# Optimization experiments

Measured on AMD Instinct MI355X. Metric: run time of the kernel, lower is better.

## Reference

```python
import jax, jax.numpy as jnp
import numpy as np

B, S, D, H = 2, 2048, 1024, 16
DK = D // H

def setup_inputs() -> dict:
    key = jax.random.key(0)
    ks = jax.random.split(key, 9)
    scale = 1.0 / np.sqrt(D)
    return {
        "x": jax.random.normal(ks[0], (B, S, D), dtype=jnp.float32),
        "Wq": jax.random.uniform(ks[1], (D, D), jnp.float32, -scale, scale),
        "bq": jax.random.uniform(ks[2], (D,), jnp.float32, -scale, scale),
        "Wk": jax.random.uniform(ks[3], (D, D), jnp.float32, -scale, scale),
        "bk": jax.random.uniform(ks[4], (D,), jnp.float32, -scale, scale),
        "Wv": jax.random.uniform(ks[5], (D, D), jnp.float32, -scale, scale),
        "bv": jax.random.uniform(ks[6], (D,), jnp.float32, -scale, scale),
        "Wo": jax.random.uniform(ks[7], (D, D), jnp.float32, -scale, scale),
        "bo": jax.random.uniform(ks[8], (D,), jnp.float32, -scale, scale),
    }

def reference(x, Wq, bq, Wk, bk, Wv, bv, Wo, bo):
    # QKV projections (torch Linear: x @ W.T + b)
    q = x @ Wq.T + bq
    k = x @ Wk.T + bk
    v = x @ Wv.T + bv
    # [B, H, S, DK]
    q = q.reshape(B, S, H, DK).transpose(0, 2, 1, 3)
    k = k.reshape(B, S, H, DK).transpose(0, 2, 1, 3)
    v = v.reshape(B, S, H, DK).transpose(0, 2, 1, 3)
    scores = jnp.einsum('bhqd,bhkd->bhqk', q, k) / jnp.sqrt(jnp.float32(DK))
    p = jax.nn.softmax(scores, axis=-1)  # dropout is identity in eval mode
    o = jnp.einsum('bhqk,bhkd->bhqd', p, v)
    o = o.transpose(0, 2, 1, 3).reshape(B, S, D)
    return o @ Wo.T + bo
```

## Files before the change

### kernel.cpp

```cpp
#include <hip/hip_runtime.h>
#include <hip/hip_bf16.h>


typedef __attribute__((ext_vector_type(8))) short short8;
typedef __attribute__((ext_vector_type(4))) float f32x4;
typedef __attribute__((ext_vector_type(4))) unsigned int u32x4;
typedef __attribute__((ext_vector_type(8))) unsigned short u16x8;

__device__ __forceinline__ unsigned short f2bf(float f) {
    unsigned int u = __builtin_bit_cast(unsigned int, f);
    u += 0x7FFFu + ((u >> 16) & 1u);
    return (unsigned short)(u >> 16);
}

__device__ __forceinline__ unsigned short bfc(float f) {
    return __builtin_bit_cast(unsigned short, __float2bfloat16(f));
}

__device__ __forceinline__ float exp2_fast(float x) {
    return __builtin_amdgcn_exp2f(x);
}

__device__ __forceinline__ void gload16(const void* gsrc, void* ldst) {
    __builtin_amdgcn_global_load_lds(
        (const __attribute__((address_space(1))) unsigned int*)gsrc,
        (__attribute__((address_space(3))) unsigned int*)ldst, 16, 0, 0);
}

__global__ void cast_all(const float* __restrict__ x,
                         const float* __restrict__ wq, const float* __restrict__ wk,
                         const float* __restrict__ wv, const float* __restrict__ wo,
                         unsigned short* __restrict__ xb,
                         unsigned short* __restrict__ wqb, unsigned short* __restrict__ wkb,
                         unsigned short* __restrict__ wvb, unsigned short* __restrict__ wob)
{
    const int bid = blockIdx.x;
    const float* src; unsigned short* dst; int i;
    if (bid < 4096) {
        src = x; dst = xb; i = bid * 256 + threadIdx.x;
    } else {
        int t = (bid - 4096) >> 10;
        int lb = (bid - 4096) & 1023;
        src = (t == 0) ? wq : (t == 1) ? wk : (t == 2) ? wv : wo;
        dst = (t == 0) ? wqb : (t == 1) ? wkb : (t == 2) ? wvb : wob;
        i = lb * 256 + threadIdx.x;
    }
    float4 v = reinterpret_cast<const float4*>(src)[i];
    ushort4 o;
    o.x = f2bf(v.x); o.y = f2bf(v.y); o.z = f2bf(v.z); o.w = f2bf(v.w);
    reinterpret_cast<ushort4*>(dst)[i] = o;
}

__global__ __launch_bounds__(256, 2)
void qkv_gemm(const unsigned short* __restrict__ A,
              const unsigned short* __restrict__ Wq_,
              const unsigned short* __restrict__ Wk_,
              const unsigned short* __restrict__ Wv_,
              const float* __restrict__ bq_,
              const float* __restrict__ bk_,
              const float* __restrict__ bv_,
              unsigned short* __restrict__ Qb,
              unsigned short* __restrict__ Kb,
              unsigned short* __restrict__ Vtb)
{
    const int K = 1024;
    __shared__ __align__(16) unsigned short As[128][64];
    __shared__ __align__(16) unsigned short Bs[128][64];

    const int lid = blockIdx.x + 8 * blockIdx.y + 256 * blockIdx.z;
    const int xcd = lid & 7;
    const int j   = lid >> 3;
    const int z   = j >> 5;
    const int rr  = j & 31;
    const int by  = xcd * 4 + (rr >> 3);
    const int bx  = rr & 7;

    const unsigned short* Bw = (z == 0) ? Wq_ : (z == 1) ? Wk_ : Wv_;
    const float* bias = (z == 0) ? bq_ : (z == 1) ? bk_ : bv_;
    unsigned short* dst = (z == 0) ? Qb : (z == 1) ? Kb : Vtb;
    const float alpha = (z == 0) ? 0.125f * 1.44269504088896340736f : 1.0f;

    const int tid  = threadIdx.x;
    const int lane = tid & 63;
    const int wave = tid >> 6;
    const int wm = (wave >> 1) * 64;
    const int wn = (wave & 1) * 64;
    const int rowBase = by * 128;
    const int colBase = bx * 128;
    const int l15 = lane & 15;
    const int lg  = lane >> 4;

    const int srow   = lane >> 3;
    const int schunk = lane & 7;
    const int gchunk = schunk ^ srow;

    f32x4 acc[4][4] = {};

    for (int kt = 0; kt < K; kt += 64) {
        __syncthreads();
#pragma unroll
        for (int it = 0; it < 4; ++it) {
            int r = wave * 8 + it * 32 + srow;
            gload16(A  + (size_t)(rowBase + r) * K + kt + gchunk * 8, &As[wave * 8 + it * 32][0]);
            gload16(Bw + (size_t)(colBase + r) * K + kt + gchunk * 8, &Bs[wave * 8 + it * 32][0]);
        }
        __syncthreads();
#pragma unroll
        for (int kk = 0; kk < 2; ++kk) {
            short8 af[4], bf[4];
#pragma unroll
            for (int fm = 0; fm < 4; ++fm) {
                int r  = wm + fm * 16 + l15;
                int kb = (kk * 4 + lg) ^ (r & 7);
                af[fm] = *reinterpret_cast<const short8*>(&As[r][kb * 8]);
            }
#pragma unroll
            for (int fn = 0; fn < 4; ++fn) {
                int r  = wn + fn * 16 + l15;
                int kb = (kk * 4 + lg) ^ (r & 7);
                bf[fn] = *reinterpret_cast<const short8*>(&Bs[r][kb * 8]);
            }
#pragma unroll
            for (int fm = 0; fm < 4; ++fm)
#pragma unroll
                for (int fn = 0; fn < 4; ++fn)
                    acc[fm][fn] = __builtin_amdgcn_mfma_f32_16x16x32_bf16(
                        af[fm], bf[fn], acc[fm][fn], 0, 0, 0);
        }
    }

#pragma unroll
    for (int fm = 0; fm < 4; ++fm)
#pragma unroll
        for (int fn = 0; fn < 4; ++fn)
#pragma unroll
            for (int r = 0; r < 4; ++r) {
                int grow = rowBase + wm + fm * 16 + lg * 4 + r;
                int gcol = colBase + wn + fn * 16 + l15;
                float v = (acc[fm][fn][r] + bias[gcol]) * alpha;
                int b = grow >> 11, s = grow & 2047;
                int h = gcol >> 6,  dk = gcol & 63;
                if (z < 2)
                    dst[(((size_t)b * 16 + h) * 2048 + s) * 64 + dk] = f2bf(v);
                else
                    dst[(((size_t)b * 16 + h) * 64 + dk) * 2048 + s] = f2bf(v);
            }
}

__global__ __launch_bounds__(256, 2)
void gemm_out(const unsigned short* __restrict__ A,
              const unsigned short* __restrict__ Bw,
              const float* __restrict__ bias,
              float* __restrict__ Cout, int M, int N, int K)
{
    __shared__ __align__(16) unsigned short As[128][64];
    __shared__ __align__(16) unsigned short Bs[64][64];

    const int lid = blockIdx.x + 16 * blockIdx.y;
    const int xcd = lid & 7;
    const int j   = lid >> 3;
    const int by  = xcd * 4 + (j >> 4);
    const int bx  = j & 15;

    const int tid  = threadIdx.x;
    const int lane = tid & 63;
    const int wave = tid >> 6;
    const int wm = (wave >> 1) * 64;
    const int wn = (wave & 1) * 32;
    const int rowBase = by * 128;
    const int colBase = bx * 64;
    const int l15 = lane & 15;
    const int lg  = lane >> 4;

    const int srow   = lane >> 3;
    const int schunk = lane & 7;
    const int gchunk = schunk ^ srow;

    f32x4 acc[4][2] = {};

    for (int kt = 0; kt < K; kt += 64) {
        __syncthreads();
#pragma unroll
        for (int it = 0; it < 4; ++it) {
            int r = wave * 8 + it * 32 + srow;
            gload16(A + (size_t)(rowBase + r) * K + kt + gchunk * 8, &As[wave * 8 + it * 32][0]);
        }
#pragma unroll
        for (int it = 0; it < 2; ++it) {
            int rb = wave * 16 + it * 8;
            int r  = rb + srow;
            gload16(Bw + (size_t)(colBase + r) * K + kt + gchunk * 8, &Bs[rb][0]);
        }
        __syncthreads();
#pragma unroll
        for (int kk = 0; kk < 2; ++kk) {
            short8 af[4], bf[2];
#pragma unroll
            for (int fm = 0; fm < 4; ++fm) {
                int r  = wm + fm * 16 + l15;
                int kb = (kk * 4 + lg) ^ (r & 7);
                af[fm] = *reinterpret_cast<const short8*>(&As[r][kb * 8]);
            }
#pragma unroll
            for (int fn = 0; fn < 2; ++fn) {
                int r  = wn + fn * 16 + l15;
                int kb = (kk * 4 + lg) ^ (r & 7);
                bf[fn] = *reinterpret_cast<const short8*>(&Bs[r][kb * 8]);
            }
#pragma unroll
            for (int fm = 0; fm < 4; ++fm)
#pragma unroll
                for (int fn = 0; fn < 2; ++fn)
                    acc[fm][fn] = __builtin_amdgcn_mfma_f32_16x16x32_bf16(
                        af[fm], bf[fn], acc[fm][fn], 0, 0, 0);
        }
    }

#pragma unroll
    for (int fm = 0; fm < 4; ++fm)
#pragma unroll
        for (int fn = 0; fn < 2; ++fn)
#pragma unroll
            for (int r = 0; r < 4; ++r) {
                int grow = rowBase + wm + fm * 16 + lg * 4 + r;
                int gcol = colBase + wn + fn * 16 + l15;
                Cout[(size_t)grow * N + gcol] = acc[fm][fn][r] + bias[gcol];
            }
}

__global__ __launch_bounds__(256, 2)
void attn_kernel(const unsigned short* __restrict__ Q,
                 const unsigned short* __restrict__ Kt,
                 const unsigned short* __restrict__ Vt,
                 unsigned short* __restrict__ O)
{
    __shared__ __align__(16) unsigned short Ks[2][128][64];
    __shared__ __align__(16) unsigned short Vs[2][64][128];

    const int lid = blockIdx.x + 16 * blockIdx.y;
    const int bh  = 4 * (lid & 7) + ((lid >> 3) & 3);
    const int qt  = lid >> 5;
    const int tid  = threadIdx.x;
    const int lane = tid & 63;
    const int w    = tid >> 6;
    const int l15 = lane & 15;
    const int lg  = lane >> 4;

    const unsigned short* Qbh = Q  + (size_t)bh * 2048 * 64;
    const unsigned short* Kbh = Kt + (size_t)bh * 2048 * 64;
    const unsigned short* Vbh = Vt + (size_t)bh * 64 * 2048;

    short8 qf[2][2];
#pragma unroll
    for (int fq = 0; fq < 2; ++fq)
#pragma unroll
        for (int kk = 0; kk < 2; ++kk) {
            int row = qt * 128 + w * 32 + fq * 16 + l15;
            qf[fq][kk] = *reinterpret_cast<const short8*>(
                Qbh + (size_t)row * 64 + kk * 32 + lg * 8);
        }

    short8 ones;
#pragma unroll
    for (int j = 0; j < 8; ++j) ones[j] = (short)0x3F80;

    f32x4 accO[2][4] = {};
    f32x4 accSum[2] = {};

    const int sr  = tid >> 3, skb = tid & 7;
    const int vr  = tid >> 4, vkb = tid & 15;

    u16x8 kst[4], vst[4];
#pragma unroll
    for (int it = 0; it < 4; ++it)
        kst[it] = *reinterpret_cast<const u16x8*>(Kbh + (size_t)(sr + it * 32) * 64 + skb * 8);
#pragma unroll
    for (int it = 0; it < 4; ++it)
        vst[it] = *reinterpret_cast<const u16x8*>(Vbh + (size_t)(vr + it * 16) * 2048 + vkb * 8);

    int cur = 0;
    for (int t = 0; t < 16; ++t) {
#pragma unroll
        for (int it = 0; it < 4; ++it) {
            int r = sr + it * 32;
            *reinterpret_cast<u16x8*>(&Ks[cur][r][(skb ^ (r & 7)) * 8]) = kst[it];
        }
#pragma unroll
        for (int it = 0; it < 4; ++it) {
            int r = vr + it * 16;
            *reinterpret_cast<u16x8*>(&Vs[cur][r][(vkb ^ (r & 15)) * 8]) = vst[it];
        }
        __syncthreads();

        if (t < 15) {
#pragma unroll
            for (int it = 0; it < 4; ++it)
                kst[it] = *reinterpret_cast<const u16x8*>(
                    Kbh + (size_t)((t + 1) * 128 + sr + it * 32) * 64 + skb * 8);
#pragma unroll
            for (int it = 0; it < 4; ++it)
                vst[it] = *reinterpret_cast<const u16x8*>(
                    Vbh + (size_t)(vr + it * 16) * 2048 + (t + 1) * 128 + vkb * 8);
        }

        f32x4 accS[8][2] = {};
#pragma unroll
        for (int kk = 0; kk < 2; ++kk) {
            short8 kf[8];
#pragma unroll
            for (int fk = 0; fk < 8; ++fk) {
                int r  = fk * 16 + l15;
                int kb = (kk * 4 + lg) ^ (r & 7);
                kf[fk] = *reinterpret_cast<const short8*>(&Ks[cur][r][kb * 8]);
            }
#pragma unroll
            for (int fk = 0; fk < 8; ++fk)
#pragma unroll
                for (int fq = 0; fq < 2; ++fq)
                    accS[fk][fq] = __builtin_amdgcn_mfma_f32_16x16x32_bf16(
                        kf[fk], qf[fq][kk], accS[fk][fq], 0, 0, 0);
        }

#pragma unroll
        for (int hh = 0; hh < 2; ++hh) {
            unsigned int plo[2][4], phi[2][4];
#pragma unroll
            for (int fq = 0; fq < 2; ++fq)
#pragma unroll
                for (int f2 = 0; f2 < 4; ++f2) {
                    int fk = hh * 4 + f2;
                    float p0 = exp2_fast(accS[fk][fq][0]);
                    float p1 = exp2_fast(accS[fk][fq][1]);
                    float p2 = exp2_fast(accS[fk][fq][2]);
                    float p3 = exp2_fast(accS[fk][fq][3]);
                    plo[fq][f2] = (unsigned int)bfc(p0) | ((unsigned int)bfc(p1) << 16);
                    phi[fq][f2] = (unsigned int)bfc(p2) | ((unsigned int)bfc(p3) << 16);
                }

#pragma unroll
            for (int k2 = 0; k2 < 2; ++k2) {
                short8 vf[4];
#pragma unroll
                for (int fd = 0; fd < 4; ++fd) {
                    int row = fd * 16 + l15;
                    int kb  = ((hh * 2 + k2) * 4 + lg) ^ (row & 15);
                    vf[fd] = *reinterpret_cast<const short8*>(&Vs[cur][row][kb * 8]);
                }
#pragma unroll
                for (int fq = 0; fq < 2; ++fq) {
                    unsigned int Alo = plo[fq][2 * k2], Blo = plo[fq][2 * k2 + 1];
                    auto r1 = __builtin_amdgcn_permlane32_swap(Alo, Blo, false, false);
                    auto r2 = __builtin_amdgcn_permlane16_swap(r1[0], r1[1], false, false);
                    unsigned int Ahi = phi[fq][2 * k2], Bhi = phi[fq][2 * k2 + 1];
                    auto r3 = __builtin_amdgcn_permlane32_swap(Ahi, Bhi, false, false);
                    auto r4 = __builtin_amdgcn_permlane16_swap(r3[0], r3[1], false, false);
                    u32x4 fw;
                    fw[0] = r2[0];
                    fw[1] = r4[0];
                    fw[2] = r2[1];
                    fw[3] = r4[1];
                    short8 pf = __builtin_bit_cast(short8, fw);
#pragma unroll
                    for (int fd = 0; fd < 4; ++fd)
                        accO[fq][fd] = __builtin_amdgcn_mfma_f32_16x16x32_bf16(
                            pf, vf[fd], accO[fq][fd], 0, 0, 0);
                    accSum[fq] = __builtin_amdgcn_mfma_f32_16x16x32_bf16(
                        pf, ones, accSum[fq], 0, 0, 0);
                }
            }
        }

        cur ^= 1;
    }

    const int b = bh >> 4, h = bh & 15;
#pragma unroll
    for (int fq = 0; fq < 2; ++fq)
#pragma unroll
        for (int r = 0; r < 4; ++r) {
            float linv = 1.0f / accSum[fq][r];
            int s = qt * 128 + w * 32 + fq * 16 + lg * 4 + r;
#pragma unroll
            for (int fd = 0; fd < 4; ++fd) {
                int dk = fd * 16 + l15;
                O[((size_t)b * 2048 + s) * 1024 + h * 64 + dk] = f2bf(accO[fq][fd][r] * linv);
            }
        }
}

extern "C" void kernel_launch(void* const* d_in, const int* in_sizes, int n_in,
                              void* d_out, int out_size, void* d_ws, size_t ws_size,
                              hipStream_t stream)
{
    const float* x  = (const float*)d_in[0];
    const float* Wq = (const float*)d_in[1];
    const float* bq = (const float*)d_in[2];
    const float* Wk = (const float*)d_in[3];
    const float* bk = (const float*)d_in[4];
    const float* Wv = (const float*)d_in[5];
    const float* bv = (const float*)d_in[6];
    const float* Wo = (const float*)d_in[7];
    const float* bo = (const float*)d_in[8];
    float* out = (float*)d_out;

    char* ws = (char*)d_ws;
    unsigned short* xb  = (unsigned short*)(ws);
    unsigned short* wqb = (unsigned short*)(ws + ((size_t)8  << 20));
    unsigned short* wkb = (unsigned short*)(ws + ((size_t)10 << 20));
    unsigned short* wvb = (unsigned short*)(ws + ((size_t)12 << 20));
    unsigned short* wob = (unsigned short*)(ws + ((size_t)14 << 20));
    unsigned short* Qb  = (unsigned short*)(ws + ((size_t)16 << 20));
    unsigned short* Kb  = (unsigned short*)(ws + ((size_t)24 << 20));
    unsigned short* Vtb = (unsigned short*)(ws + ((size_t)32 << 20));
    unsigned short* Ob  = (unsigned short*)(ws + ((size_t)40 << 20));

    cast_all<<<8192, 256, 0, stream>>>(x, Wq, Wk, Wv, Wo,
                                       xb, wqb, wkb, wvb, wob);

    qkv_gemm<<<dim3(8, 32, 3), 256, 0, stream>>>(xb, wqb, wkb, wvb, bq, bk, bv,
                                                 Qb, Kb, Vtb);

    attn_kernel<<<dim3(16, 32), 256, 0, stream>>>(Qb, Kb, Vtb, Ob);

    gemm_out<<<dim3(16, 32), 256, 0, stream>>>(Ob, wob, bo, out, 4096, 1024, 1024);
}
```

Baseline: 109.0 us.

## Software-pipeline attention loop so PV of previous tile overlaps QK^T of current

The attention main loop is restructured so each step computes QK^T and the exp/pack for key tile t while running the P·V MFMAs for tile t-1, using ping-pong register buffers for the packed probabilities. The goal is to interleave the exp (transcendental) work with independent MFMA work so the matrix units stay busy instead of waiting on the softmax. The cost is doubled P register storage, which adds register pressure and may lower occupancy, plus an extra barrier per step to protect the double-buffered LDS.

```diff
diff --git a/kernel.cpp b/kernel.cpp
--- a/kernel.cpp
+++ b/kernel.cpp
@@ -266,112 +266,149 @@
 
     f32x4 accO[2][4] = {};
     f32x4 accSum[2] = {};
+    f32x4 accS[8][2];
 
     const int sr  = tid >> 3, skb = tid & 7;
     const int vr  = tid >> 4, vkb = tid & 15;
 
     u16x8 kst[4], vst[4];
-#pragma unroll
-    for (int it = 0; it < 4; ++it)
-        kst[it] = *reinterpret_cast<const u16x8*>(Kbh + (size_t)(sr + it * 32) * 64 + skb * 8);
-#pragma unroll
-    for (int it = 0; it < 4; ++it)
-        vst[it] = *reinterpret_cast<const u16x8*>(Vbh + (size_t)(vr + it * 16) * 2048 + vkb * 8);
-
-    int cur = 0;
-    for (int t = 0; t < 16; ++t) {
-#pragma unroll
-        for (int it = 0; it < 4; ++it) {
-            int r = sr + it * 32;
-            *reinterpret_cast<u16x8*>(&Ks[cur][r][(skb ^ (r & 7)) * 8]) = kst[it];
-        }
-#pragma unroll
-        for (int it = 0; it < 4; ++it) {
-            int r = vr + it * 16;
-            *reinterpret_cast<u16x8*>(&Vs[cur][r][(vkb ^ (r & 15)) * 8]) = vst[it];
-        }
-        __syncthreads();
-
-        if (t < 15) {
-#pragma unroll
-            for (int it = 0; it < 4; ++it)
-                kst[it] = *reinterpret_cast<const u16x8*>(
-                    Kbh + (size_t)((t + 1) * 128 + sr + it * 32) * 64 + skb * 8);
-#pragma unroll
-            for (int it = 0; it < 4; ++it)
-                vst[it] = *reinterpret_cast<const u16x8*>(
-                    Vbh + (size_t)(vr + it * 16) * 2048 + (t + 1) * 128 + vkb * 8);
-        }
-
-        f32x4 accS[8][2] = {};
-#pragma unroll
-        for (int kk = 0; kk < 2; ++kk) {
-            short8 kf[8];
-#pragma unroll
-            for (int fk = 0; fk < 8; ++fk) {
-                int r  = fk * 16 + l15;
-                int kb = (kk * 4 + lg) ^ (r & 7);
-                kf[fk] = *reinterpret_cast<const short8*>(&Ks[cur][r][kb * 8]);
-            }
-#pragma unroll
-            for (int fk = 0; fk < 8; ++fk)
-#pragma unroll
-                for (int fq = 0; fq < 2; ++fq)
-                    accS[fk][fq] = __builtin_amdgcn_mfma_f32_16x16x32_bf16(
-                        kf[fk], qf[fq][kk], accS[fk][fq], 0, 0, 0);
-        }
-
-#pragma unroll
-        for (int hh = 0; hh < 2; ++hh) {
-            unsigned int plo[2][4], phi[2][4];
-#pragma unroll
-            for (int fq = 0; fq < 2; ++fq)
-#pragma unroll
-                for (int f2 = 0; f2 < 4; ++f2) {
-                    int fk = hh * 4 + f2;
-                    float p0 = exp2_fast(accS[fk][fq][0]);
-                    float p1 = exp2_fast(accS[fk][fq][1]);
-                    float p2 = exp2_fast(accS[fk][fq][2]);
-                    float p3 = exp2_fast(accS[fk][fq][3]);
-                    plo[fq][f2] = (unsigned int)bfc(p0) | ((unsigned int)bfc(p1) << 16);
-                    phi[fq][f2] = (unsigned int)bfc(p2) | ((unsigned int)bfc(p3) << 16);
-                }
-
-#pragma unroll
-            for (int k2 = 0; k2 < 2; ++k2) {
-                short8 vf[4];
-#pragma unroll
-                for (int fd = 0; fd < 4; ++fd) {
-                    int row = fd * 16 + l15;
-                    int kb  = ((hh * 2 + k2) * 4 + lg) ^ (row & 15);
-                    vf[fd] = *reinterpret_cast<const short8*>(&Vs[cur][row][kb * 8]);
-                }
-#pragma unroll
-                for (int fq = 0; fq < 2; ++fq) {
-                    unsigned int Alo = plo[fq][2 * k2], Blo = plo[fq][2 * k2 + 1];
-                    auto r1 = __builtin_amdgcn_permlane32_swap(Alo, Blo, false, false);
-                    auto r2 = __builtin_amdgcn_permlane16_swap(r1[0], r1[1], false, false);
-                    unsigned int Ahi = phi[fq][2 * k2], Bhi = phi[fq][2 * k2 + 1];
-                    auto r3 = __builtin_amdgcn_permlane32_swap(Ahi, Bhi, false, false);
-                    auto r4 = __builtin_amdgcn_permlane16_swap(r3[0], r3[1], false, false);
-                    u32x4 fw;
-                    fw[0] = r2[0];
-                    fw[1] = r4[0];
-                    fw[2] = r2[1];
-                    fw[3] = r4[1];
-                    short8 pf = __builtin_bit_cast(short8, fw);
-#pragma unroll
-                    for (int fd = 0; fd < 4; ++fd)
-                        accO[fq][fd] = __builtin_amdgcn_mfma_f32_16x16x32_bf16(
-                            pf, vf[fd], accO[fq][fd], 0, 0, 0);
-                    accSum[fq] = __builtin_amdgcn_mfma_f32_16x16x32_bf16(
-                        pf, ones, accSum[fq], 0, 0, 0);
-                }
-            }
-        }
-
-        cur ^= 1;
-    }
+    unsigned int PAlo[2][2][4], PAhi[2][2][4];
+    unsigned int PBlo[2][2][4], PBhi[2][2][4];
+
+#define GLOAD(T)                                                              \
+    {                                                                         \
+        _Pragma("unroll")                                                     \
+        for (int it = 0; it < 4; ++it)                                        \
+            kst[it] = *reinterpret_cast<const u16x8*>(                        \
+                Kbh + (size_t)((T) * 128 + sr + it * 32) * 64 + skb * 8);     \
+        _Pragma("unroll")                                                     \
+        for (int it = 0; it < 4; ++it)                                        \
+            vst[it] = *reinterpret_cast<const u16x8*>(                        \
+                Vbh + (size_t)(vr + it * 16) * 2048 + (T) * 128 + vkb * 8);   \
+    }
+
+#define WRITE_T(BT)                                                           \
+    {                                                                         \
+        _Pragma("unroll")                                                     \
+        for (int it = 0; it < 4; ++it) {                                      \
+            int r = sr + it * 32;                                             \
+            *reinterpret_cast<u16x8*>(&Ks[BT][r][(skb ^ (r & 7)) * 8]) = kst[it]; \
+        }                                                                     \
+        _Pragma("unroll")                                                     \
+        for (int it = 0; it < 4; ++it) {                                      \
+            int r = vr + it * 16;                                             \
+            *reinterpret_cast<u16x8*>(&Vs[BT][r][(vkb ^ (r & 15)) * 8]) = vst[it]; \
+        }                                                                     \
+    }
+
+#define QKT_T(BT)                                                             \
+    {                                                                         \
+        _Pragma("unroll")                                                     \
+        for (int fk = 0; fk < 8; ++fk)                                        \
+            _Pragma("unroll")                                                 \
+            for (int fq = 0; fq < 2; ++fq) accS[fk][fq] = f32x4{};            \
+        _Pragma("unroll")                                                     \
+        for (int kk = 0; kk < 2; ++kk) {                                      \
+            short8 kf[8];                                                     \
+            _Pragma("unroll")                                                 \
+            for (int fk = 0; fk < 8; ++fk) {                                  \
+                int r  = fk * 16 + l15;                                       \
+                int kb = (kk * 4 + lg) ^ (r & 7);                             \
+                kf[fk] = *reinterpret_cast<const short8*>(&Ks[BT][r][kb * 8]);\
+            }                                                                 \
+            _Pragma("unroll")                                                 \
+            for (int fk = 0; fk < 8; ++fk)                                    \
+                _Pragma("unroll")                                             \
+                for (int fq = 0; fq < 2; ++fq)                                \
+                    accS[fk][fq] = __builtin_amdgcn_mfma_f32_16x16x32_bf16(   \
+                        kf[fk], qf[fq][kk], accS[fk][fq], 0, 0, 0);           \
+        }                                                                     \
+    }
+
+#define PACK_T(PClo, PChi)                                                    \
+    {                                                                         \
+        _Pragma("unroll")                                                     \
+        for (int hh = 0; hh < 2; ++hh)                                        \
+            _Pragma("unroll")                                                 \
+            for (int fq = 0; fq < 2; ++fq)                                    \
+                _Pragma("unroll")                                             \
+                for (int f2 = 0; f2 < 4; ++f2) {                              \
+                    int fk = hh * 4 + f2;                                     \
+                    float p0 = exp2_fast(accS[fk][fq][0]);                    \
+                    float p1 = exp2_fast(accS[fk][fq][1]);                    \
+                    float p2 = exp2_fast(accS[fk][fq][2]);                    \
+                    float p3 = exp2_fast(accS[fk][fq][3]);                    \
+                    PClo[hh][fq][f2] = (unsigned int)bfc(p0) | ((unsigned int)bfc(p1) << 16); \
+                    PChi[hh][fq][f2] = (unsigned int)bfc(p2) | ((unsigned int)bfc(p3) << 16); \
+                }                                                             \
+    }
+
+#define PV_PREV(BV, PPlo, PPhi)                                               \
+    {                                                                         \
+        _Pragma("unroll")                                                     \
+        for (int hh = 0; hh < 2; ++hh)                                        \
+            _Pragma("unroll")                                                 \
+            for (int k2 = 0; k2 < 2; ++k2) {                                  \
+                short8 vf[4];                                                 \
+                _Pragma("unroll")                                             \
+                for (int fd = 0; fd < 4; ++fd) {                              \
+                    int row = fd * 16 + l15;                                  \
+                    int kb  = ((hh * 2 + k2) * 4 + lg) ^ (row & 15);          \
+                    vf[fd] = *reinterpret_cast<const short8*>(&Vs[BV][row][kb * 8]); \
+                }                                                             \
+                _Pragma("unroll")                                             \
+                for (int fq = 0; fq < 2; ++fq) {                              \
+                    unsigned int Alo = PPlo[hh][fq][2 * k2], Blo = PPlo[hh][fq][2 * k2 + 1]; \
+                    auto r1 = __builtin_amdgcn_permlane32_swap(Alo, Blo, false, false); \
+                    auto r2 = __builtin_amdgcn_permlane16_swap(r1[0], r1[1], false, false); \
+                    unsigned int Ahi = PPhi[hh][fq][2 * k2], Bhi = PPhi[hh][fq][2 * k2 + 1]; \
+                    auto r3 = __builtin_amdgcn_permlane32_swap(Ahi, Bhi, false, false); \
+                    auto r4 = __builtin_amdgcn_permlane16_swap(r3[0], r3[1], false, false); \
+                    u32x4 fw;                                                 \
+                    fw[0] = r2[0]; fw[1] = r4[0]; fw[2] = r2[1]; fw[3] = r4[1]; \
+                    short8 pf = __builtin_bit_cast(short8, fw);               \
+                    _Pragma("unroll")                                         \
+                    for (int fd = 0; fd < 4; ++fd)                            \
+                        accO[fq][fd] = __builtin_amdgcn_mfma_f32_16x16x32_bf16( \
+                            pf, vf[fd], accO[fq][fd], 0, 0, 0);               \
+                    accSum[fq] = __builtin_amdgcn_mfma_f32_16x16x32_bf16(     \
+                        pf, ones, accSum[fq], 0, 0, 0);                       \
+                }                                                             \
+            }                                                                 \
+    }
+
+#define STEP(T, BT, PPlo, PPhi, PClo, PChi)                                   \
+    {                                                                         \
+        WRITE_T(BT);                                                          \
+        __syncthreads();                                                      \
+        if ((T) < 15) { GLOAD((T) + 1); }                                     \
+        QKT_T(BT);                                                            \
+        PV_PREV(BT ^ 1, PPlo, PPhi);                                          \
+        PACK_T(PClo, PChi);                                                   \
+        __syncthreads();                                                      \
+    }
+
+    GLOAD(0);
+    WRITE_T(0);
+    __syncthreads();
+    GLOAD(1);
+    QKT_T(0);
+    PACK_T(PAlo, PAhi);
+    __syncthreads();
+
+    for (int base = 1; base < 15; base += 2) {
+        STEP(base,     1, PAlo, PAhi, PBlo, PBhi);
+        STEP(base + 1, 0, PBlo, PBhi, PAlo, PAhi);
+    }
+    STEP(15, 1, PAlo, PAhi, PBlo, PBhi);
+    PV_PREV(1, PBlo, PBhi);
+
+#undef GLOAD
+#undef WRITE_T
+#undef QKT_T
+#undef PACK_T
+#undef PV_PREV
+#undef STEP
 
     const int b = bh >> 4, h = bh & 15;
 #pragma unroll
```

Result: no change. 108.9 us, median of 2 (-0.1%).
